# Optimization experiments

Measured on AMD Instinct MI355X. Metric: run time of the kernel, lower is better.

The kernel has to match this reference:

```python
import jax, jax.numpy as jnp
import numpy as np

OUT = 7            # output_size
SR = 2             # sampling_ratio (samples per bin per axis)
SCALES = (0.25, 0.125, 0.0625, 0.03125)
CANON_SIZE = 224.0
CANON_LVL = 4.0
MIN_LVL = 2
IMG = 800.0


def setup_inputs() -> dict:
    key = jax.random.key(0)
    kf = jax.random.split(key, 6)
    B, C, R = 2, 256, 256
    sizes = [200, 100, 50, 25]
    feats = [jax.random.normal(kf[i], (B, C, s, s), jnp.float32) for i, s in enumerate(sizes)]
    # valid xyxy boxes in [0, IMG], log-uniform side lengths -> spread across FPN levels
    ctr = jax.random.uniform(kf[4], (B, R, 2), minval=0.0, maxval=IMG)
    wh = jnp.exp(jax.random.uniform(kf[5], (B, R, 2), minval=float(np.log(16.0)), maxval=float(np.log(512.0))))
    lo = jnp.clip(ctr - wh / 2, 0.0, IMG)
    hi = jnp.clip(ctr + wh / 2, 0.0, IMG)
    boxes = jnp.concatenate([lo, hi], axis=-1)  # [B,R,4]
    return {"feat0": feats[0], "feat1": feats[1], "feat2": feats[2], "feat3": feats[3], "boxes": boxes}


def _prep(c, lim):
    """torchvision ROIAlign (aligned=False) bilinear index prep.
    c: sample coords [N,OUT,SR]; lim: per-box feature extent (H or W) [N]."""
    limb = lim[:, None, None]
    valid = (c > -1.0) & (c < limb)          # out-of-range samples contribute 0
    cc = jnp.maximum(c, 0.0)
    low = jnp.floor(cc)
    cap = limb - 1.0
    at_edge = low >= cap                      # y_low >= H-1 -> clamp, frac = 0
    low = jnp.minimum(low, cap)
    high = jnp.minimum(low + 1.0, cap)
    cc = jnp.where(at_edge, low, cc)
    frac = cc - low
    return valid, low.astype(jnp.int32), high.astype(jnp.int32), frac


def roi_pooler(feats, boxes):
    B, R = boxes.shape[0], boxes.shape[1]
    C = feats[0].shape[1]
    N = B * R
    flat = boxes.reshape(N, 4)
    bidx = jnp.repeat(jnp.arange(B, dtype=jnp.int32), R)  # batch index per ROI

    # level assignment (assign_boxes_to_levels)
    area = (flat[:, 2] - flat[:, 0]) * (flat[:, 3] - flat[:, 1])
    lvl = jnp.floor(CANON_LVL + jnp.log2(jnp.sqrt(area) / CANON_SIZE + 1e-8))
    lvl = jnp.clip(lvl, MIN_LVL, MIN_LVL + len(feats) - 1).astype(jnp.int32) - MIN_LVL  # [N] in [0,3]

    # pad all levels to P2 size and stack so each ROI is sampled once at its level
    Hm, Wm = feats[0].shape[2], feats[0].shape[3]
    padded = jnp.stack([jnp.pad(f, ((0, 0), (0, 0), (0, Hm - f.shape[2]), (0, Wm - f.shape[3]))) for f in feats])
    fp = padded.transpose(0, 1, 3, 4, 2)  # [L,B,Hm,Wm,C] channels-last for gather
    Hs = jnp.array([f.shape[2] for f in feats], jnp.float32)[lvl]
    Ws = jnp.array([f.shape[3] for f in feats], jnp.float32)[lvl]
    scale = jnp.array(SCALES, jnp.float32)[lvl]

    # ROIAlign aligned=False: scale coords, clamp roi size to >= 1
    x1 = flat[:, 0] * scale
    y1 = flat[:, 1] * scale
    x2 = flat[:, 2] * scale
    y2 = flat[:, 3] * scale
    roi_w = jnp.maximum(x2 - x1, 1.0)
    roi_h = jnp.maximum(y2 - y1, 1.0)
    bw = roi_w / OUT
    bh = roi_h / OUT

    # sample grid: bin index + sub-sample offsets -> [N,OUT,SR]
    grid = jnp.arange(OUT, dtype=jnp.float32)[None, :, None] + (jnp.arange(SR, dtype=jnp.float32)[None, None, :] + 0.5) / SR
    ys = y1[:, None, None] + bh[:, None, None] * grid
    xs = x1[:, None, None] + bw[:, None, None] * grid

    vy, yl, yh, fy = _prep(ys, Hs)
    vx, xl, xh, fx = _prep(xs, Ws)

    P = OUT * OUT * SR * SR  # all sample points per ROI

    def by(a):  # y-axis quantity -> broadcast over (out_y,out_x,sr_y,sr_x)
        return jnp.broadcast_to(a[:, :, None, :, None], (N, OUT, OUT, SR, SR)).reshape(N, P)

    def bx(a):
        return jnp.broadcast_to(a[:, None, :, None, :], (N, OUT, OUT, SR, SR)).reshape(N, P)

    YL, YH, FY, VY = by(yl), by(yh), by(fy), by(vy)
    XL, XH, FX, VX = bx(xl), bx(xh), bx(fx), bx(vx)

    li = lvl[:, None]
    bi = bidx[:, None]
    v00 = fp[li, bi, YL, XL]  # [N,P,C]
    v01 = fp[li, bi, YL, XH]
    v10 = fp[li, bi, YH, XL]
    v11 = fp[li, bi, YH, XH]

    w = lambda a: a[..., None]
    val = (w((1 - FY) * (1 - FX)) * v00 + w((1 - FY) * FX) * v01
           + w(FY * (1 - FX)) * v10 + w(FY * FX) * v11)
    val = val * w((VY & VX).astype(val.dtype))
    out = val.reshape(N, OUT, OUT, SR * SR, C).mean(axis=3)  # average over SR*SR samples
    return out.transpose(0, 3, 1, 2)  # [N,C,OUT,OUT]


def reference(feat0, feat1, feat2, feat3, boxes):
    return roi_pooler([feat0, feat1, feat2, feat3], boxes)
```

## Files before the change

### kernel.cpp

```cpp
#include <hip/hip_runtime.h>
#include <math.h>

typedef unsigned short u16;
typedef unsigned int   u32;

#define OUTSZ 7
#define B_ 2
#define C_ 256
#define R_ 256
#define N_ (B_ * R_)

#define PX_TOTAL 106250
#define WS_NEEDED ((size_t)PX_TOTAL * 256 * 2)

__device__ __forceinline__ u16 f2bf(float v) {
    u32 u = __float_as_uint(v);
    u += 0x7fffu + ((u >> 16) & 1u);
    return (u16)(u >> 16);
}

__device__ __forceinline__ u32 pack2bf(float a, float b) {
    return (u32)f2bf(a) | ((u32)f2bf(b) << 16);
}

__global__ __launch_bounds__(512, 8) void nhwc_cast(
    const float* __restrict__ f0, const float* __restrict__ f1,
    const float* __restrict__ f2, const float* __restrict__ f3,
    u16* __restrict__ dst)
{
    __shared__ u32 lds32[256 * 32];
    const int tid  = threadIdx.x;
    const int lane = tid & 63;
    const int wave = tid >> 6;

    const int t  = blockIdx.x;
    const int cb = blockIdx.y;
    const int b  = blockIdx.z;
    const float* src; int HWsz, dstBase, ft;
    if      (t < 157) { src = f0; HWsz = 40000; dstBase = 0;      ft = t;       }
    else if (t < 197) { src = f1; HWsz = 10000; dstBase = 80000;  ft = t - 157; }
    else if (t < 207) { src = f2; HWsz = 2500;  dstBase = 100000; ft = t - 197; }
    else              { src = f3; HWsz = 625;   dstBase = 105000; ft = t - 207; }

    const int fbase = ft * 256;
    const int cw    = cb * 64 + wave * 8;
    const int rem   = HWsz - fbase;
    const int p0    = 4 * lane;
    const bool vec  = ((HWsz & 3) == 0) && (p0 + 3 < rem);

    const float* base = src + ((size_t)(b * C_ + cw)) * HWsz + fbase;

    float f[8][4];
    #pragma unroll
    for (int i = 0; i < 8; ++i) {
        const float* row = base + (size_t)i * HWsz;
        if (vec) {
            float4 v = *(const float4*)(row + p0);
            f[i][0] = v.x; f[i][1] = v.y; f[i][2] = v.z; f[i][3] = v.w;
        } else {
            #pragma unroll
            for (int k = 0; k < 4; ++k)
                f[i][k] = (p0 + k < rem) ? row[p0 + k] : 0.0f;
        }
    }
    __builtin_amdgcn_sched_barrier(0);

    #pragma unroll
    for (int j = 0; j < 4; ++j) {
        uint4 o;
        o.x = pack2bf(f[0][j], f[1][j]);
        o.y = pack2bf(f[2][j], f[3][j]);
        o.z = pack2bf(f[4][j], f[5][j]);
        o.w = pack2bf(f[6][j], f[7][j]);
        const int q = wave ^ (lane & 7);
        *(uint4*)&lds32[(p0 + j) * 32 + q * 4] = o;
    }
    __syncthreads();

    const int maxpx = rem < 256 ? rem : 256;
    #pragma unroll
    for (int i = 0; i < 4; ++i) {
        const int idx = i * 512 + tid;
        const int px  = idx >> 3;
        const int sub = idx & 7;
        if (px < maxpx) {
            const int q = sub ^ ((px >> 2) & 7);
            uint4 o = *(const uint4*)&lds32[px * 32 + q * 4];
            *(uint4*)(dst + (size_t)(dstBase + b * HWsz + fbase + px) * 256 + cb * 64 + sub * 8) = o;
        }
    }
}

__global__ __launch_bounds__(512, 8) void roi_gather(
    const u16* __restrict__ ws16, const float* __restrict__ boxes,
    float* __restrict__ out)
{
    __shared__ float lds[128 * 49];
    __shared__ float s_wy0[14], s_wy1[14], s_wx0[14], s_wx1[14];
    __shared__ int   s_yl[14], s_yh[14], s_xl[14], s_xh[14];
    __shared__ int   s_base, s_W;

    const int g    = blockIdx.x;
    const int n    = blockIdx.y;
    const int tid  = threadIdx.x;
    const int lane = tid & 63;
    const int wave = tid >> 6;

    if (tid < 28) {
        const float* bx = boxes + (size_t)n * 4;
        float x1 = bx[0], y1 = bx[1], x2 = bx[2], y2 = bx[3];
        float area = (x2 - x1) * (y2 - y1);
        float lf = floorf(4.0f + log2f(sqrtf(area) / 224.0f + 1e-8f));
        lf = fminf(fmaxf(lf, 2.0f), 5.0f);
        int lvl = (int)lf - 2;
        const float scales[4] = {0.25f, 0.125f, 0.0625f, 0.03125f};
        const int   sizes[4]  = {200, 100, 50, 25};
        const int   bases[4]  = {0, 80000, 100000, 105000};
        float scale = scales[lvl];
        int   HW    = sizes[lvl];
        float lim = (float)HW, cap = lim - 1.0f;
        float fx1 = x1 * scale, fy1 = y1 * scale;
        float bw = fmaxf(x2 * scale - fx1, 1.0f) / (float)OUTSZ;
        float bh = fmaxf(y2 * scale - fy1, 1.0f) / (float)OUTSZ;
        if (tid == 0) { s_base = bases[lvl] + (n >> 8) * HW * HW; s_W = HW; }

        const int  i   = (tid < 14) ? tid : tid - 14;
        const bool isy = tid < 14;
        float o  = isy ? fy1 : fx1;
        float st = isy ? bh  : bw;
        float gq = (float)(i >> 1) + ((float)(i & 1) + 0.5f) * 0.5f;
        float c = o + st * gq;
        bool  v = (c > -1.0f) && (c < lim);
        float cc = fmaxf(c, 0.0f);
        float low = floorf(cc);
        bool  edge = low >= cap;
        low = fminf(low, cap);
        float high = fminf(low + 1.0f, cap);
        float fr = edge ? 0.0f : (cc - low);
        float w0 = v ? (1.0f - fr) : 0.0f;
        float w1 = v ? fr : 0.0f;
        if (isy) { s_yl[i] = (int)low; s_yh[i] = (int)high; s_wy0[i] = w0; s_wy1[i] = w1; }
        else     { s_xl[i] = (int)low; s_xh[i] = (int)high; s_wx0[i] = w0; s_wx1[i] = w1; }
    }
    __syncthreads();

    const int base = s_base, W = s_W;
    const int c0 = g * 128;

    for (int cell = wave; cell < 49; cell += 8) {
        const int cu = __builtin_amdgcn_readfirstlane(cell);
        const int oy = cu / 7, ox = cu - oy * 7;
        float a0 = 0.0f, a1 = 0.0f;
        #pragma unroll
        for (int sy = 0; sy < 2; ++sy) {
            const int ei = oy * 2 + sy;
            const float wy0 = s_wy0[ei], wy1 = s_wy1[ei];
            const int rl = base + s_yl[ei] * W;
            const int rh = base + s_yh[ei] * W;
            #pragma unroll
            for (int sx = 0; sx < 2; ++sx) {
                const int ej = ox * 2 + sx;
                const float w00 = wy0 * s_wx0[ej], w01 = wy0 * s_wx1[ej];
                const float w10 = wy1 * s_wx0[ej], w11 = wy1 * s_wx1[ej];
                const int xl = s_xl[ej], xh = s_xh[ej];
                u32 u00 = ((const u32*)(ws16 + (size_t)(rl + xl) * 256 + c0))[lane];
                u32 u01 = ((const u32*)(ws16 + (size_t)(rl + xh) * 256 + c0))[lane];
                u32 u10 = ((const u32*)(ws16 + (size_t)(rh + xl) * 256 + c0))[lane];
                u32 u11 = ((const u32*)(ws16 + (size_t)(rh + xh) * 256 + c0))[lane];
                a0 += w00 * __uint_as_float(u00 << 16) + w01 * __uint_as_float(u01 << 16)
                    + w10 * __uint_as_float(u10 << 16) + w11 * __uint_as_float(u11 << 16);
                a1 += w00 * __uint_as_float(u00 & 0xffff0000u) + w01 * __uint_as_float(u01 & 0xffff0000u)
                    + w10 * __uint_as_float(u10 & 0xffff0000u) + w11 * __uint_as_float(u11 & 0xffff0000u);
            }
        }
        lds[(2 * lane) * 49 + cu]     = a0 * 0.25f;
        lds[(2 * lane + 1) * 49 + cu] = a1 * 0.25f;
    }
    __syncthreads();

    const float4* lv = (const float4*)lds;
    float4* ov = (float4*)(out + ((size_t)(n * C_ + c0)) * 49);
    for (int i = tid; i < 1568; i += 512) ov[i] = lv[i];
}

__global__ __launch_bounds__(256) void roi_direct(
    const float* __restrict__ f0, const float* __restrict__ f1,
    const float* __restrict__ f2, const float* __restrict__ f3,
    const float* __restrict__ boxes, float* __restrict__ out)
{
    const int total = B_ * R_ * C_ * OUTSZ * OUTSZ;
    int idx = blockIdx.x * blockDim.x + threadIdx.x;
    if (idx >= total) return;
    int ox = idx % 7, oy = (idx / 7) % 7, c = (idx / 49) % C_, n = idx / (49 * C_), b = n >> 8;
    const float* bx = boxes + (size_t)n * 4;
    float x1 = bx[0], y1 = bx[1], x2 = bx[2], y2 = bx[3];
    float lf = floorf(4.0f + log2f(sqrtf((x2 - x1) * (y2 - y1)) / 224.0f + 1e-8f));
    int lvl = (int)fminf(fmaxf(lf, 2.0f), 5.0f) - 2;
    const float scales[4] = {0.25f, 0.125f, 0.0625f, 0.03125f};
    const int sizes[4] = {200, 100, 50, 25};
    float scale = scales[lvl]; int HW = sizes[lvl];
    const float* fl = lvl == 0 ? f0 : lvl == 1 ? f1 : lvl == 2 ? f2 : f3;
    float fx1 = x1 * scale, fy1 = y1 * scale;
    float bw = fmaxf(x2 * scale - fx1, 1.0f) / 7.0f, bh = fmaxf(y2 * scale - fy1, 1.0f) / 7.0f;
    const float* plane = fl + ((size_t)(b * C_ + c)) * HW * HW;
    float lim = (float)HW, cap = lim - 1.0f, acc = 0.0f;
    #pragma unroll
    for (int sy = 0; sy < 2; sy++) {
        float yc = fy1 + bh * ((float)oy + ((float)sy + 0.5f) * 0.5f);
        bool vy = (yc > -1.0f) && (yc < lim);
        float ccy = fmaxf(yc, 0.0f), lowy = floorf(ccy);
        bool ey = lowy >= cap; lowy = fminf(lowy, cap);
        float highy = fminf(lowy + 1.0f, cap);
        float wfy = ey ? 0.0f : (ccy - lowy);
        int yl = (int)lowy, yh = (int)highy;
        #pragma unroll
        for (int sx = 0; sx < 2; sx++) {
            float xc = fx1 + bw * ((float)ox + ((float)sx + 0.5f) * 0.5f);
            bool vx = (xc > -1.0f) && (xc < lim);
            float ccx = fmaxf(xc, 0.0f), lowx = floorf(ccx);
            bool ex = lowx >= cap; lowx = fminf(lowx, cap);
            float highx = fminf(lowx + 1.0f, cap);
            float wfx = ex ? 0.0f : (ccx - lowx);
            int xl = (int)lowx, xh = (int)highx;
            if (vy && vx) {
                float v00 = plane[yl * HW + xl], v01 = plane[yl * HW + xh];
                float v10 = plane[yh * HW + xl], v11 = plane[yh * HW + xh];
                acc += (1.0f - wfy) * ((1.0f - wfx) * v00 + wfx * v01)
                     + wfy * ((1.0f - wfx) * v10 + wfx * v11);
            }
        }
    }
    out[idx] = acc * 0.25f;
}

extern "C" void kernel_launch(void* const* d_in, const int* in_sizes, int n_in,
                              void* d_out, int out_size, void* d_ws, size_t ws_size,
                              hipStream_t stream) {
    const float* f0    = (const float*)d_in[0];
    const float* f1    = (const float*)d_in[1];
    const float* f2    = (const float*)d_in[2];
    const float* f3    = (const float*)d_in[3];
    const float* boxes = (const float*)d_in[4];
    float* out = (float*)d_out;

    if (ws_size < WS_NEEDED) {
        const int total = B_ * R_ * C_ * OUTSZ * OUTSZ;
        roi_direct<<<(total + 255) / 256, 256, 0, stream>>>(f0, f1, f2, f3, boxes, out);
        return;
    }

    u16* nhwc = (u16*)d_ws;

    nhwc_cast<<<dim3(210, 4, 2), 512, 0, stream>>>(f0, f1, f2, f3, nhwc);
    roi_gather<<<dim3(2, N_), 512, 0, stream>>>(nhwc, boxes, out);
}
```

Measured before the change: 177.9 us.

## Retile NHWC bf16 cast kernel to 64-pixel by full-channel tiles

Restructures the NCHW-to-NHWC bf16 conversion so each block handles 64 pixels across all 256 channels instead of 256 pixels across 64 channels. Each thread now reads two channel rows and packs them into bf16 pairs in a swizzled LDS tile. Each output pixel record of 512 bytes is then written contiguously by 8 threads. The aim is fully contiguous global writes and a different grid shape with more, smaller blocks, at the cost of shorter contiguous read runs per channel row.

```diff
diff --git a/kernel.cpp b/kernel.cpp
--- a/kernel.cpp
+++ b/kernel.cpp
@@ -23,70 +23,73 @@
     return (u32)f2bf(a) | ((u32)f2bf(b) << 16);
 }
 
-__global__ __launch_bounds__(512, 8) void nhwc_cast(
+__global__ __launch_bounds__(512) void nhwc_cast(
     const float* __restrict__ f0, const float* __restrict__ f1,
     const float* __restrict__ f2, const float* __restrict__ f3,
     u16* __restrict__ dst)
 {
-    __shared__ u32 lds32[256 * 32];
-    const int tid  = threadIdx.x;
-    const int lane = tid & 63;
-    const int wave = tid >> 6;
-
-    const int t  = blockIdx.x;
-    const int cb = blockIdx.y;
-    const int b  = blockIdx.z;
+    __shared__ u32 sm[64 * 128];
+    const int tid = threadIdx.x;
+
+    const int t = blockIdx.x;
+    const int b = blockIdx.y;
     const float* src; int HWsz, dstBase, ft;
-    if      (t < 157) { src = f0; HWsz = 40000; dstBase = 0;      ft = t;       }
-    else if (t < 197) { src = f1; HWsz = 10000; dstBase = 80000;  ft = t - 157; }
-    else if (t < 207) { src = f2; HWsz = 2500;  dstBase = 100000; ft = t - 197; }
-    else              { src = f3; HWsz = 625;   dstBase = 105000; ft = t - 207; }
-
-    const int fbase = ft * 256;
-    const int cw    = cb * 64 + wave * 8;
-    const int rem   = HWsz - fbase;
-    const int p0    = 4 * lane;
-    const bool vec  = ((HWsz & 3) == 0) && (p0 + 3 < rem);
-
-    const float* base = src + ((size_t)(b * C_ + cw)) * HWsz + fbase;
-
-    float f[8][4];
-    #pragma unroll
-    for (int i = 0; i < 8; ++i) {
-        const float* row = base + (size_t)i * HWsz;
-        if (vec) {
-            float4 v = *(const float4*)(row + p0);
-            f[i][0] = v.x; f[i][1] = v.y; f[i][2] = v.z; f[i][3] = v.w;
-        } else {
+    if      (t < 625) { src = f0; HWsz = 40000; dstBase = 0;      ft = t;       }
+    else if (t < 782) { src = f1; HWsz = 10000; dstBase = 80000;  ft = t - 625; }
+    else if (t < 822) { src = f2; HWsz = 2500;  dstBase = 100000; ft = t - 782; }
+    else              { src = f3; HWsz = 625;   dstBase = 105000; ft = t - 822; }
+
+    const int px0 = ft * 64;
+    const int rem = HWsz - px0;
+    const int p   = tid >> 2;
+    const int qb  = tid & 3;
+
+    const float* r0 = src + (size_t)(b * C_ + 2 * p) * HWsz + px0;
+    const float* r1 = r0 + HWsz;
+    const bool vec = ((HWsz & 3) == 0) && (rem >= 64);
+
+    if (vec) {
+        #pragma unroll
+        for (int i = 0; i < 4; ++i) {
+            const int q = i * 4 + qb;
+            float4 v0 = *(const float4*)(r0 + 4 * q);
+            float4 v1 = *(const float4*)(r1 + 4 * q);
             #pragma unroll
-            for (int k = 0; k < 4; ++k)
-                f[i][k] = (p0 + k < rem) ? row[p0 + k] : 0.0f;
-        }
-    }
-    __builtin_amdgcn_sched_barrier(0);
-
-    #pragma unroll
-    for (int j = 0; j < 4; ++j) {
-        uint4 o;
-        o.x = pack2bf(f[0][j], f[1][j]);
-        o.y = pack2bf(f[2][j], f[3][j]);
-        o.z = pack2bf(f[4][j], f[5][j]);
-        o.w = pack2bf(f[6][j], f[7][j]);
-        const int q = wave ^ (lane & 7);
-        *(uint4*)&lds32[(p0 + j) * 32 + q * 4] = o;
+            for (int j = 0; j < 4; ++j) {
+                const int px = 4 * q + j;
+                const int idx = px * 128 + (((p >> 2) ^ (px & 7)) << 2) + (p & 3);
+                float a = j == 0 ? v0.x : j == 1 ? v0.y : j == 2 ? v0.z : v0.w;
+                float c = j == 0 ? v1.x : j == 1 ? v1.y : j == 2 ? v1.z : v1.w;
+                sm[idx] = pack2bf(a, c);
+            }
+        }
+    } else {
+        #pragma unroll
+        for (int i = 0; i < 4; ++i) {
+            const int q = i * 4 + qb;
+            #pragma unroll
+            for (int j = 0; j < 4; ++j) {
+                const int px = 4 * q + j;
+                float a = (px < rem) ? r0[px] : 0.0f;
+                float c = (px < rem) ? r1[px] : 0.0f;
+                const int idx = px * 128 + (((p >> 2) ^ (px & 7)) << 2) + (p & 3);
+                sm[idx] = pack2bf(a, c);
+            }
+        }
     }
     __syncthreads();
 
-    const int maxpx = rem < 256 ? rem : 256;
-    #pragma unroll
-    for (int i = 0; i < 4; ++i) {
-        const int idx = i * 512 + tid;
-        const int px  = idx >> 3;
-        const int sub = idx & 7;
-        if (px < maxpx) {
-            const int q = sub ^ ((px >> 2) & 7);
-            uint4 o = *(const uint4*)&lds32[px * 32 + q * 4];
-            *(uint4*)(dst + (size_t)(dstBase + b * HWsz + fbase + px) * 256 + cb * 64 + sub * 8) = o;
+    const int px  = tid >> 3;
+    const int sub = tid & 7;
+    if (px < rem) {
+        u16* rec = dst + (size_t)(dstBase + b * HWsz + px0 + px) * 256;
+        const u32* row = &sm[px * 128];
+        #pragma unroll
+        for (int i = 0; i < 4; ++i) {
+            const int c  = i * 8 + sub;
+            const int pc = c ^ (px & 7);
+            uint4 o = *(const uint4*)&row[pc << 2];
+            *(uint4*)(rec + (c << 3)) = o;
         }
     }
 }
@@ -251,6 +254,6 @@
 
     u16* nhwc = (u16*)d_ws;
 
-    nhwc_cast<<<dim3(210, 4, 2), 512, 0, stream>>>(f0, f1, f2, f3, nhwc);
+    nhwc_cast<<<dim3(832, 2), 512, 0, stream>>>(f0, f1, f2, f3, nhwc);
     roi_gather<<<dim3(2, N_), 512, 0, stream>>>(nhwc, boxes, out);
 }
```

After: 187.8 us. 5.6% more time.

## Gather adjacent x-pixel pairs with one 16-byte load per row in ROI gather

Applied to the files above, without the earlier changes.

The ROI gather kernel now runs one block per ROI over all 256 channels instead of two 128-channel blocks. Each lane loads a uint4 covering the two horizontally adjacent pixels (xl and xl+1) for 8 channels, so the lower and upper half-waves carry the x-low and x-high taps. The halves are combined with a cross-half shuffle, and edge columns are handled by shifting the offset and folding the weights. Output goes through a padded transposed LDS buffer, and a sched_barrier in the cast kernel is removed. The aim is fewer, wider global loads per bilinear sample. In exchange it adds shuffle traffic, a larger LDS footprint and scattered LDS reads in the store loop.

```diff
diff --git a/kernel.cpp b/kernel.cpp
--- a/kernel.cpp
+++ b/kernel.cpp
@@ -22,6 +22,9 @@
 __device__ __forceinline__ u32 pack2bf(float a, float b) {
     return (u32)f2bf(a) | ((u32)f2bf(b) << 16);
 }
+
+__device__ __forceinline__ float bflo(u32 u) { return __uint_as_float(u << 16); }
+__device__ __forceinline__ float bfhi(u32 u) { return __uint_as_float(u & 0xffff0000u); }
 
 __global__ __launch_bounds__(512, 8) void nhwc_cast(
     const float* __restrict__ f0, const float* __restrict__ f1,
@@ -63,7 +66,6 @@
                 f[i][k] = (p0 + k < rem) ? row[p0 + k] : 0.0f;
         }
     }
-    __builtin_amdgcn_sched_barrier(0);
 
     #pragma unroll
     for (int j = 0; j < 4; ++j) {
@@ -91,17 +93,16 @@
     }
 }
 
-__global__ __launch_bounds__(512, 8) void roi_gather(
+__global__ __launch_bounds__(512) void roi_gather(
     const u16* __restrict__ ws16, const float* __restrict__ boxes,
     float* __restrict__ out)
 {
-    __shared__ float lds[128 * 49];
-    __shared__ float s_wy0[14], s_wy1[14], s_wx0[14], s_wx1[14];
-    __shared__ int   s_yl[14], s_yh[14], s_xl[14], s_xh[14];
+    __shared__ float ldsO[49 * 264];
+    __shared__ float s_wy0[14], s_wy1[14], s_wlo[14], s_whi[14];
+    __shared__ int   s_yl[14], s_yh[14], s_xo[14];
     __shared__ int   s_base, s_W;
 
-    const int g    = blockIdx.x;
-    const int n    = blockIdx.y;
+    const int n    = blockIdx.x;
     const int tid  = threadIdx.x;
     const int lane = tid & 63;
     const int wave = tid >> 6;
@@ -139,48 +140,71 @@
         float fr = edge ? 0.0f : (cc - low);
         float w0 = v ? (1.0f - fr) : 0.0f;
         float w1 = v ? fr : 0.0f;
-        if (isy) { s_yl[i] = (int)low; s_yh[i] = (int)high; s_wy0[i] = w0; s_wy1[i] = w1; }
-        else     { s_xl[i] = (int)low; s_xh[i] = (int)high; s_wx0[i] = w0; s_wx1[i] = w1; }
+        if (isy) {
+            s_yl[i] = (int)low; s_yh[i] = (int)high; s_wy0[i] = w0; s_wy1[i] = w1;
+        } else {
+            int xl = (int)low, xh = (int)high;
+            bool col = (xh == xl);
+            s_xo[i]  = col ? xl - 1 : xl;
+            s_wlo[i] = col ? 0.0f : w0;
+            s_whi[i] = col ? (w0 + w1) : w1;
+        }
     }
     __syncthreads();
 
     const int base = s_base, W = s_W;
-    const int c0 = g * 128;
+    const bool hiHalf = lane >= 32;
 
     for (int cell = wave; cell < 49; cell += 8) {
         const int cu = __builtin_amdgcn_readfirstlane(cell);
         const int oy = cu / 7, ox = cu - oy * 7;
-        float a0 = 0.0f, a1 = 0.0f;
+        float a0 = 0, a1 = 0, a2 = 0, a3 = 0, a4 = 0, a5 = 0, a6 = 0, a7 = 0;
         #pragma unroll
         for (int sy = 0; sy < 2; ++sy) {
             const int ei = oy * 2 + sy;
             const float wy0 = s_wy0[ei], wy1 = s_wy1[ei];
-            const int rl = base + s_yl[ei] * W;
-            const int rh = base + s_yh[ei] * W;
+            const size_t rl = (size_t)(base + s_yl[ei] * W);
+            const size_t rh = (size_t)(base + s_yh[ei] * W);
             #pragma unroll
             for (int sx = 0; sx < 2; ++sx) {
                 const int ej = ox * 2 + sx;
-                const float w00 = wy0 * s_wx0[ej], w01 = wy0 * s_wx1[ej];
-                const float w10 = wy1 * s_wx0[ej], w11 = wy1 * s_wx1[ej];
-                const int xl = s_xl[ej], xh = s_xh[ej];
-                u32 u00 = ((const u32*)(ws16 + (size_t)(rl + xl) * 256 + c0))[lane];
-                u32 u01 = ((const u32*)(ws16 + (size_t)(rl + xh) * 256 + c0))[lane];
-                u32 u10 = ((const u32*)(ws16 + (size_t)(rh + xl) * 256 + c0))[lane];
-                u32 u11 = ((const u32*)(ws16 + (size_t)(rh + xh) * 256 + c0))[lane];
-                a0 += w00 * __uint_as_float(u00 << 16) + w01 * __uint_as_float(u01 << 16)
-                    + w10 * __uint_as_float(u10 << 16) + w11 * __uint_as_float(u11 << 16);
-                a1 += w00 * __uint_as_float(u00 & 0xffff0000u) + w01 * __uint_as_float(u01 & 0xffff0000u)
-                    + w10 * __uint_as_float(u10 & 0xffff0000u) + w11 * __uint_as_float(u11 & 0xffff0000u);
+                const int xo = s_xo[ej];
+                const float wsel = hiHalf ? s_whi[ej] : s_wlo[ej];
+                uint4 A = ((const uint4*)(ws16 + (rl + xo) * 256))[lane];
+                const float wa = wy0 * wsel;
+                a0 += wa * bflo(A.x); a1 += wa * bfhi(A.x);
+                a2 += wa * bflo(A.y); a3 += wa * bfhi(A.y);
+                a4 += wa * bflo(A.z); a5 += wa * bfhi(A.z);
+                a6 += wa * bflo(A.w); a7 += wa * bfhi(A.w);
+                uint4 Bv = ((const uint4*)(ws16 + (rh + xo) * 256))[lane];
+                const float wb = wy1 * wsel;
+                a0 += wb * bflo(Bv.x); a1 += wb * bfhi(Bv.x);
+                a2 += wb * bflo(Bv.y); a3 += wb * bfhi(Bv.y);
+                a4 += wb * bflo(Bv.z); a5 += wb * bfhi(Bv.z);
+                a6 += wb * bflo(Bv.w); a7 += wb * bfhi(Bv.w);
             }
         }
-        lds[(2 * lane) * 49 + cu]     = a0 * 0.25f;
-        lds[(2 * lane + 1) * 49 + cu] = a1 * 0.25f;
+        a0 += __shfl_xor(a0, 32); a1 += __shfl_xor(a1, 32);
+        a2 += __shfl_xor(a2, 32); a3 += __shfl_xor(a3, 32);
+        a4 += __shfl_xor(a4, 32); a5 += __shfl_xor(a5, 32);
+        a6 += __shfl_xor(a6, 32); a7 += __shfl_xor(a7, 32);
+        float* dstl = &ldsO[cu * 264 + (lane & 31) * 8 + (hiHalf ? 4 : 0)];
+        float4 v = hiHalf ? make_float4(a4 * 0.25f, a5 * 0.25f, a6 * 0.25f, a7 * 0.25f)
+                          : make_float4(a0 * 0.25f, a1 * 0.25f, a2 * 0.25f, a3 * 0.25f);
+        *(float4*)dstl = v;
     }
     __syncthreads();
 
-    const float4* lv = (const float4*)lds;
-    float4* ov = (float4*)(out + ((size_t)(n * C_ + c0)) * 49);
-    for (int i = tid; i < 1568; i += 512) ov[i] = lv[i];
+    float* op = out + (size_t)n * (C_ * 49);
+    for (int i4 = tid; i4 < 3136; i4 += 512) {
+        const int e = 4 * i4;
+        float4 v;
+        {   int c = e / 49,      r = e - 49 * c;          v.x = ldsO[r * 264 + c]; }
+        {   int c = (e+1) / 49,  r = (e+1) - 49 * c;      v.y = ldsO[r * 264 + c]; }
+        {   int c = (e+2) / 49,  r = (e+2) - 49 * c;      v.z = ldsO[r * 264 + c]; }
+        {   int c = (e+3) / 49,  r = (e+3) - 49 * c;      v.w = ldsO[r * 264 + c]; }
+        *(float4*)(op + e) = v;
+    }
 }
 
 __global__ __launch_bounds__(256) void roi_direct(
@@ -252,5 +276,5 @@
     u16* nhwc = (u16*)d_ws;
 
     nhwc_cast<<<dim3(210, 4, 2), 512, 0, stream>>>(f0, f1, f2, f3, nhwc);
-    roi_gather<<<dim3(2, N_), 512, 0, stream>>>(nhwc, boxes, out);
-}
+    roi_gather<<<dim3(N_), 512, 0, stream>>>(nhwc, boxes, out);
+}
```

Result: no change. 180.5 us (+1.5%).
